# Performance work log

Hardware: AMD Instinct MI355X
Metric: run time of the kernel (lower is better)

## Reference

```python
import jax, jax.numpy as jnp
import numpy as np

F_FACETS = 400000
TEX_PER = 4            # textures per facet (counts sum must equal total textures)
T_TEX = F_FACETS * TEX_PER
C_IN = 64
C_OUT = 64
L = 2
N_BASIS = (L + 1) ** 2  # 9
BN_EPS = 1e-3


def setup_inputs() -> dict:
    key = jax.random.key(0)
    k1, k2, k3 = jax.random.split(key, 3)
    input_texture = jax.random.normal(k1, (T_TEX, C_IN), jnp.float32)
    bary_coeff = jax.random.uniform(k2, (T_TEX, N_BASIS), jnp.float32)
    # per-facet texture counts; constant 4 so counts sum exactly to T_TEX
    num_texture = jnp.full((F_FACETS,), TEX_PER, dtype=jnp.int32)
    # xavier_normal_ on [O, I, K]: fan_in = I*K, fan_out = ... torch uses fan_in=I*K? For 3D it treats dim1*rest.
    std = float(np.sqrt(2.0 / (C_IN * N_BASIS + C_OUT * N_BASIS)))
    weights = jax.random.normal(k3, (C_OUT, C_IN, N_BASIS), jnp.float32) * std
    biases = jnp.zeros((1, C_OUT), jnp.float32)
    gamma = jnp.ones((C_OUT,), jnp.float32)
    beta = jnp.zeros((C_OUT,), jnp.float32)
    return {
        "input_texture": input_texture,
        "bary_coeff": bary_coeff,
        "weights": weights,
        "biases": biases,
        "gamma": gamma,
        "beta": beta,
        "num_texture": num_texture,
    }


def reference(input_texture, bary_coeff, weights, biases, gamma, beta, num_texture):
    T = input_texture.shape[0]
    n_facets = num_texture.shape[0]
    n_basis = weights.shape[2]
    # per-texture contribution: contrib[t,o] = sum_{i,k} x[t,i] * W[o,i,k] * bary[t,k]
    # loop over small fixed basis count (9) to avoid a [T, I, K] intermediate
    contrib = jnp.zeros((T, weights.shape[0]), dtype=input_texture.dtype)
    for k in range(n_basis):
        contrib = contrib + (input_texture @ weights[:, :, k].T) * bary_coeff[:, k:k + 1]
    # scatter-sum per facet (ragged groups given by num_texture), then average
    seg_ids = jnp.repeat(jnp.arange(n_facets), num_texture, total_repeat_length=T)
    facet_sum = jax.ops.segment_sum(contrib, seg_ids, num_segments=n_facets)
    out = facet_sum / num_texture[:, None].astype(facet_sum.dtype)
    # bias + ReLU
    out = jax.nn.relu(out + biases)
    # BatchNorm1d in training mode: batch stats (biased variance), eps=1e-3
    mu = jnp.mean(out, axis=0)
    var = jnp.mean(jnp.square(out - mu), axis=0)
    out = (out - mu) * jax.lax.rsqrt(var + BN_EPS) * gamma + beta
    return out
```

## Files before the change

kernel.cpp:

```cpp
#include <hip/hip_runtime.h>


typedef _Float16 half8  __attribute__((ext_vector_type(8)));
typedef _Float16 h2     __attribute__((ext_vector_type(2)));
typedef __fp16   fp16x2 __attribute__((ext_vector_type(2)));
typedef float    f32x4  __attribute__((ext_vector_type(4)));
typedef float    f32x4u __attribute__((ext_vector_type(4), aligned(4)));

#define NGROUPS 100000
#define FFACETS 400000
#define GRID1   1024

union HF { h2 h[4]; half8 v; };

static __device__ __forceinline__ h2 pkrtz(float a, float b) {
    fp16x2 r = __builtin_amdgcn_cvt_pkrtz(a, b);
    return __builtin_bit_cast(h2, r);
}

__global__ __launch_bounds__(256) void prep_kernel(const float* __restrict__ W,
                                                   _Float16* __restrict__ wswz,
                                                   float* __restrict__ stats) {
    int idx = blockIdx.x * 256 + threadIdx.x;
    if (idx < 36864) {
        int j    = idx & 7;
        int lane = (idx >> 3) & 63;
        int mt   = (idx >> 9) & 3;
        int c    = idx >> 11;
        int o    = mt * 16 + (lane & 15);
        int i    = (c & 1) * 32 + ((lane >> 4) << 3) + j;
        int kb   = c >> 1;
        wswz[idx] = (_Float16)W[(o * 64 + i) * 9 + kb];
    }
    if (idx < 128) stats[idx] = 0.0f;
}

__global__ __launch_bounds__(256, 2) void pass1_kernel(
    const float* __restrict__ X, const float* __restrict__ BARY,
    const _Float16* __restrict__ WSWZ, const float* __restrict__ BIAS,
    const int* __restrict__ NTEX, float* __restrict__ OUT,
    float* __restrict__ stats) {

    __shared__ float sl_s[64];
    __shared__ float sl_s2[64];

    const int tid  = threadIdx.x;
    const int wave = tid >> 6;
    const int lane = tid & 63;
    const int col  = lane & 15;
    const int quad = lane >> 4;

    half8 wf[18];
#pragma unroll
    for (int c = 0; c < 18; ++c)
        wf[c] = *(const half8*)(WSWZ + ((size_t)(c * 4 + wave) * 64 + lane) * 8);

    const f32x4 biasv = *(const f32x4*)(BIAS + wave * 16 + quad * 4);

    float sacc[4]  = {0.f, 0.f, 0.f, 0.f};
    float s2acc[4] = {0.f, 0.f, 0.f, 0.f};

    int g = blockIdx.x;

    f32x4  x0, x1, x2, x3;
    f32x4u b0, b1;
    float  b8;
    int    nt;
    {
        const int t = g * 16 + col;
        const float* xp = X + (size_t)t * 64 + quad * 8;
        x0 = *(const f32x4*)(xp);
        x1 = *(const f32x4*)(xp + 4);
        x2 = *(const f32x4*)(xp + 32);
        x3 = *(const f32x4*)(xp + 36);
        const float* bp = BARY + (size_t)t * 9;
        b0 = *(const f32x4u*)(bp);
        b1 = *(const f32x4u*)(bp + 4);
        b8 = bp[8];
        nt = NTEX[g * 4 + (col >> 2)];
    }

    while (g < NGROUPS) {
        h2 xh[8], bh[9];
        xh[0] = pkrtz(x0[0], x0[1]);  xh[1] = pkrtz(x0[2], x0[3]);
        xh[2] = pkrtz(x1[0], x1[1]);  xh[3] = pkrtz(x1[2], x1[3]);
        xh[4] = pkrtz(x2[0], x2[1]);  xh[5] = pkrtz(x2[2], x2[3]);
        xh[6] = pkrtz(x3[0], x3[1]);  xh[7] = pkrtz(x3[2], x3[3]);
        bh[0] = pkrtz(b0[0], b0[0]);  bh[1] = pkrtz(b0[1], b0[1]);
        bh[2] = pkrtz(b0[2], b0[2]);  bh[3] = pkrtz(b0[3], b0[3]);
        bh[4] = pkrtz(b1[0], b1[0]);  bh[5] = pkrtz(b1[1], b1[1]);
        bh[6] = pkrtz(b1[2], b1[2]);  bh[7] = pkrtz(b1[3], b1[3]);
        bh[8] = pkrtz(b8, b8);
        const float rc = __builtin_amdgcn_rcpf((float)nt);
        const int gcur = g;

        g += GRID1;
        if (g < NGROUPS) {
            const int t = g * 16 + col;
            const float* xp = X + (size_t)t * 64 + quad * 8;
            x0 = *(const f32x4*)(xp);
            x1 = *(const f32x4*)(xp + 4);
            x2 = *(const f32x4*)(xp + 32);
            x3 = *(const f32x4*)(xp + 36);
            const float* bp = BARY + (size_t)t * 9;
            b0 = *(const f32x4u*)(bp);
            b1 = *(const f32x4u*)(bp + 4);
            b8 = bp[8];
            nt = NTEX[g * 4 + (col >> 2)];
        }

        f32x4 acc0 = {0.f, 0.f, 0.f, 0.f};
        f32x4 acc1 = {0.f, 0.f, 0.f, 0.f};
        __builtin_amdgcn_s_setprio(1);
#pragma unroll
        for (int c = 0; c < 18; c += 2) {
            const h2 bk = bh[c >> 1];
            HF bf0, bf1;
            bf0.h[0] = xh[0] * bk;
            bf0.h[1] = xh[1] * bk;
            bf0.h[2] = xh[2] * bk;
            bf0.h[3] = xh[3] * bk;
            acc0 = __builtin_amdgcn_mfma_f32_16x16x32_f16(wf[c], bf0.v, acc0, 0, 0, 0);
            bf1.h[0] = xh[4] * bk;
            bf1.h[1] = xh[5] * bk;
            bf1.h[2] = xh[6] * bk;
            bf1.h[3] = xh[7] * bk;
            acc1 = __builtin_amdgcn_mfma_f32_16x16x32_f16(wf[c + 1], bf1.v, acc1, 0, 0, 0);
        }
        __builtin_amdgcn_s_setprio(0);

        const int f = gcur * 4 + (col >> 2);
        f32x4 vv;
#pragma unroll
        for (int r = 0; r < 4; ++r) {
            float s = acc0[r] + acc1[r];
            s += __shfl_xor(s, 1);
            s += __shfl_xor(s, 2);
            s = s * rc + biasv[r];
            s = s > 0.f ? s : 0.f;
            vv[r] = s;
            sacc[r]  += s;
            s2acc[r] += s * s;
        }
        if ((col & 3) == 0)
            *(f32x4*)(OUT + (size_t)f * 64 + wave * 16 + quad * 4) = vv;
    }

#pragma unroll
    for (int r = 0; r < 4; ++r) {
        float s = sacc[r], s2 = s2acc[r];
        s  += __shfl_xor(s, 1);  s  += __shfl_xor(s, 2);
        s  += __shfl_xor(s, 4);  s  += __shfl_xor(s, 8);
        s2 += __shfl_xor(s2, 1); s2 += __shfl_xor(s2, 2);
        s2 += __shfl_xor(s2, 4); s2 += __shfl_xor(s2, 8);
        if (col == 0) {
            sl_s [wave * 16 + quad * 4 + r] = s  * 0.25f;
            sl_s2[wave * 16 + quad * 4 + r] = s2 * 0.25f;
        }
    }
    __syncthreads();
    if (tid < 64)        atomicAdd(&stats[tid],      sl_s [tid]);
    else if (tid < 128)  atomicAdd(&stats[tid],      sl_s2[tid - 64]);
}

__global__ __launch_bounds__(256) void pass3_kernel(float* __restrict__ OUT,
    const float* __restrict__ stats, const float* __restrict__ gamma,
    const float* __restrict__ beta) {
    const int tid = threadIdx.x;
    const size_t l = (size_t)blockIdx.x * 256 + tid;
    const int c0 = ((int)l & 15) * 4;
    float mu[4], sc[4], be[4];
    const float invF = 1.0f / (float)FFACETS;
#pragma unroll
    for (int u = 0; u < 4; ++u) {
        int ch = c0 + u;
        float m  = stats[ch] * invF;
        float va = stats[64 + ch] * invF - m * m;
        mu[u] = m;
        sc[u] = rsqrtf(va + 1e-3f) * gamma[ch];
        be[u] = beta[ch];
    }
    const size_t n4 = (size_t)FFACETS * 16;
    for (size_t i = l; i < n4; i += (size_t)gridDim.x * 256) {
        f32x4 v = ((f32x4*)OUT)[i];
#pragma unroll
        for (int u = 0; u < 4; ++u)
            v[u] = (v[u] - mu[u]) * sc[u] + be[u];
        ((f32x4*)OUT)[i] = v;
    }
}

extern "C" void kernel_launch(void* const* d_in, const int* in_sizes, int n_in,
                              void* d_out, int out_size, void* d_ws, size_t ws_size,
                              hipStream_t stream) {
    const float* X     = (const float*)d_in[0];
    const float* BARY  = (const float*)d_in[1];
    const float* W     = (const float*)d_in[2];
    const float* BIAS  = (const float*)d_in[3];
    const float* GAMMA = (const float*)d_in[4];
    const float* BETA  = (const float*)d_in[5];
    const int*   NTEX  = (const int*)d_in[6];
    float* OUT = (float*)d_out;

    _Float16* wswz = (_Float16*)d_ws;
    float* stats   = (float*)((char*)d_ws + 73728);

    prep_kernel<<<144, 256, 0, stream>>>(W, wswz, stats);
    pass1_kernel<<<GRID1, 256, 0, stream>>>(X, BARY, wswz, BIAS, NTEX, OUT, stats);
    pass3_kernel<<<2048, 256, 0, stream>>>(OUT, stats, GAMMA, BETA);
}
```

Before: 742.9 us.

## Stage X and bary tiles through LDS with async global_load_lds double buffering

Replaces the register prefetch of the next group with direct global-to-LDS async loads (global_load_lds) into a two-slot LDS ring, using a swizzled layout to avoid bank conflicts and manual vmcnt waits to keep two groups in flight. The grid shrinks to 768 blocks and the occupancy hint rises to 3 blocks per CU, since activations no longer sit in prefetch registers. The aim is more memory-level parallelism and coalesced 16-byte loads of the bary/ntex data. It adds two barriers per iteration and relies on hand-counted waitcnt values and on n being at least 2 per block.

```diff
diff --git a/kernel.cpp b/kernel.cpp
--- a/kernel.cpp
+++ b/kernel.cpp
@@ -5,17 +5,25 @@
 typedef _Float16 h2     __attribute__((ext_vector_type(2)));
 typedef __fp16   fp16x2 __attribute__((ext_vector_type(2)));
 typedef float    f32x4  __attribute__((ext_vector_type(4)));
-typedef float    f32x4u __attribute__((ext_vector_type(4), aligned(4)));
 
 #define NGROUPS 100000
 #define FFACETS 400000
-#define GRID1   1024
+#define GRID1   768
+#define LDSBUF  8192
+
+#define WAITV(N) asm volatile("s_waitcnt vmcnt(" #N ")" ::: "memory")
+#define FENCE()  asm volatile("" ::: "memory")
 
 union HF { h2 h[4]; half8 v; };
 
 static __device__ __forceinline__ h2 pkrtz(float a, float b) {
     fp16x2 r = __builtin_amdgcn_cvt_pkrtz(a, b);
     return __builtin_bit_cast(h2, r);
+}
+
+static __device__ __forceinline__ void gload16(const void* g, void* l) {
+    __builtin_amdgcn_global_load_lds((const __attribute__((address_space(1))) void*)g,
+                                     (__attribute__((address_space(3))) void*)l, 16, 0, 0);
 }
 
 __global__ __launch_bounds__(256) void prep_kernel(const float* __restrict__ W,
@@ -35,12 +43,13 @@
     if (idx < 128) stats[idx] = 0.0f;
 }
 
-__global__ __launch_bounds__(256, 2) void pass1_kernel(
+__global__ __launch_bounds__(256, 3) void pass1_kernel(
     const float* __restrict__ X, const float* __restrict__ BARY,
     const _Float16* __restrict__ WSWZ, const float* __restrict__ BIAS,
     const int* __restrict__ NTEX, float* __restrict__ OUT,
     float* __restrict__ stats) {
 
+    __shared__ __align__(16) char lds[2][LDSBUF];
     __shared__ float sl_s[64];
     __shared__ float sl_s2[64];
 
@@ -57,57 +66,57 @@
 
     const f32x4 biasv = *(const f32x4*)(BIAS + wave * 16 + quad * 4);
 
+    const int pphys  = (wave << 10) + (lane << 4);
+    const int xsoff  = pphys ^ (((pphys >> 8) & 7) << 4);
+    const char* Xb   = (const char*)X;
+    const char* BNb  = (lane < 36) ? ((const char*)BARY + lane * 16) : (const char*)NTEX;
+
+    const int m    = (col & 7) << 4;
+    const int a00  = (col << 8) + ((quad << 5) ^ m);
+    const int a10  = (col << 8) + (((quad << 5) | 16) ^ m);
+    const int bco  = 4096 + col * 36;
+    const int nco  = 4096 + 576 + ((col >> 2) << 2);
+
     float sacc[4]  = {0.f, 0.f, 0.f, 0.f};
     float s2acc[4] = {0.f, 0.f, 0.f, 0.f};
 
-    int g = blockIdx.x;
-
-    f32x4  x0, x1, x2, x3;
-    f32x4u b0, b1;
-    float  b8;
-    int    nt;
-    {
-        const int t = g * 16 + col;
-        const float* xp = X + (size_t)t * 64 + quad * 8;
-        x0 = *(const f32x4*)(xp);
-        x1 = *(const f32x4*)(xp + 4);
-        x2 = *(const f32x4*)(xp + 32);
-        x3 = *(const f32x4*)(xp + 36);
-        const float* bp = BARY + (size_t)t * 9;
-        b0 = *(const f32x4u*)(bp);
-        b1 = *(const f32x4u*)(bp + 4);
-        b8 = bp[8];
-        nt = NTEX[g * 4 + (col >> 2)];
-    }
-
-    while (g < NGROUPS) {
+    const int b = blockIdx.x;
+    const int n = (NGROUPS - 1 - b) / GRID1 + 1;
+
+    auto STAGE = [&](int p, int g) {
+        gload16(Xb + (size_t)g * 4096 + xsoff, &lds[p][pphys]);
+        if (lane < 37) {
+            size_t so = (lane < 36) ? (size_t)g * 576 : (size_t)g * 16;
+            gload16(BNb + so, &lds[p][4096 + lane * 16]);
+        }
+    };
+
+    auto ITER = [&](int p, int g, int gpre, bool do_stage) {
+        __builtin_amdgcn_s_barrier();
+        FENCE();
+        f32x4 r00 = *(const f32x4*)&lds[p][a00];
+        f32x4 r10 = *(const f32x4*)&lds[p][a10];
+        f32x4 r01 = *(const f32x4*)&lds[p][a00 + 128];
+        f32x4 r11 = *(const f32x4*)&lds[p][a10 + 128];
+        float bF[9];
+#pragma unroll
+        for (int k = 0; k < 9; ++k) bF[k] = *(const float*)&lds[p][bco + k * 4];
+        const int nt = *(const int*)&lds[p][nco];
+        asm volatile("s_waitcnt lgkmcnt(0)" ::: "memory");
+        __builtin_amdgcn_sched_barrier(0);
+        __builtin_amdgcn_s_barrier();
+        FENCE();
+        if (do_stage) STAGE(p, gpre);
+        FENCE();
+
         h2 xh[8], bh[9];
-        xh[0] = pkrtz(x0[0], x0[1]);  xh[1] = pkrtz(x0[2], x0[3]);
-        xh[2] = pkrtz(x1[0], x1[1]);  xh[3] = pkrtz(x1[2], x1[3]);
-        xh[4] = pkrtz(x2[0], x2[1]);  xh[5] = pkrtz(x2[2], x2[3]);
-        xh[6] = pkrtz(x3[0], x3[1]);  xh[7] = pkrtz(x3[2], x3[3]);
-        bh[0] = pkrtz(b0[0], b0[0]);  bh[1] = pkrtz(b0[1], b0[1]);
-        bh[2] = pkrtz(b0[2], b0[2]);  bh[3] = pkrtz(b0[3], b0[3]);
-        bh[4] = pkrtz(b1[0], b1[0]);  bh[5] = pkrtz(b1[1], b1[1]);
-        bh[6] = pkrtz(b1[2], b1[2]);  bh[7] = pkrtz(b1[3], b1[3]);
-        bh[8] = pkrtz(b8, b8);
+        xh[0] = pkrtz(r00[0], r00[1]);  xh[1] = pkrtz(r00[2], r00[3]);
+        xh[2] = pkrtz(r10[0], r10[1]);  xh[3] = pkrtz(r10[2], r10[3]);
+        xh[4] = pkrtz(r01[0], r01[1]);  xh[5] = pkrtz(r01[2], r01[3]);
+        xh[6] = pkrtz(r11[0], r11[1]);  xh[7] = pkrtz(r11[2], r11[3]);
+#pragma unroll
+        for (int k = 0; k < 9; ++k) bh[k] = pkrtz(bF[k], bF[k]);
         const float rc = __builtin_amdgcn_rcpf((float)nt);
-        const int gcur = g;
-
-        g += GRID1;
-        if (g < NGROUPS) {
-            const int t = g * 16 + col;
-            const float* xp = X + (size_t)t * 64 + quad * 8;
-            x0 = *(const f32x4*)(xp);
-            x1 = *(const f32x4*)(xp + 4);
-            x2 = *(const f32x4*)(xp + 32);
-            x3 = *(const f32x4*)(xp + 36);
-            const float* bp = BARY + (size_t)t * 9;
-            b0 = *(const f32x4u*)(bp);
-            b1 = *(const f32x4u*)(bp + 4);
-            b8 = bp[8];
-            nt = NTEX[g * 4 + (col >> 2)];
-        }
 
         f32x4 acc0 = {0.f, 0.f, 0.f, 0.f};
         f32x4 acc1 = {0.f, 0.f, 0.f, 0.f};
@@ -116,20 +125,16 @@
         for (int c = 0; c < 18; c += 2) {
             const h2 bk = bh[c >> 1];
             HF bf0, bf1;
-            bf0.h[0] = xh[0] * bk;
-            bf0.h[1] = xh[1] * bk;
-            bf0.h[2] = xh[2] * bk;
-            bf0.h[3] = xh[3] * bk;
+            bf0.h[0] = xh[0] * bk;  bf0.h[1] = xh[1] * bk;
+            bf0.h[2] = xh[2] * bk;  bf0.h[3] = xh[3] * bk;
             acc0 = __builtin_amdgcn_mfma_f32_16x16x32_f16(wf[c], bf0.v, acc0, 0, 0, 0);
-            bf1.h[0] = xh[4] * bk;
-            bf1.h[1] = xh[5] * bk;
-            bf1.h[2] = xh[6] * bk;
-            bf1.h[3] = xh[7] * bk;
+            bf1.h[0] = xh[4] * bk;  bf1.h[1] = xh[5] * bk;
+            bf1.h[2] = xh[6] * bk;  bf1.h[3] = xh[7] * bk;
             acc1 = __builtin_amdgcn_mfma_f32_16x16x32_f16(wf[c + 1], bf1.v, acc1, 0, 0, 0);
         }
         __builtin_amdgcn_s_setprio(0);
 
-        const int f = gcur * 4 + (col >> 2);
+        const int f = g * 4 + (col >> 2);
         f32x4 vv;
 #pragma unroll
         for (int r = 0; r < 4; ++r) {
@@ -144,7 +149,19 @@
         }
         if ((col & 3) == 0)
             *(f32x4*)(OUT + (size_t)f * 64 + wave * 16 + quad * 4) = vv;
-    }
+    };
+
+    STAGE(0, b);
+    STAGE(1, b + GRID1);
+    WAITV(2); ITER(0, b,         b + 2 * GRID1, true);
+    WAITV(3); ITER(1, b + GRID1, b + 3 * GRID1, true);
+    int t = 2;
+    for (; t < n - 2; ++t) {
+        WAITV(4);
+        ITER(t & 1, b + t * GRID1, b + (t + 2) * GRID1, true);
+    }
+    WAITV(4); ITER(t & 1, b + t * GRID1, 0, false); ++t;
+    WAITV(0); ITER(t & 1, b + t * GRID1, 0, false);
 
 #pragma unroll
     for (int r = 0; r < 4; ++r) {
```

Measured after the change: 687.9 us. 7.4% less time.
